# Kernel optimization log

Measured on AMD Instinct MI355X. Metric: run time of the kernel, lower is better.

The kernel has to match this reference:

```python
import jax, jax.numpy as jnp
import numpy as np

NUM_CAPSULE = 32
DIM_CAPSULE = 32
ROUTINGS = 3
T_EPSILON = 1e-7


def setup_inputs() -> dict:
    key = jax.random.key(0)
    k1, k2 = jax.random.split(key)
    x = jax.random.normal(k1, (64, 1024, 256), dtype=jnp.float32)
    # xavier_normal_ on [1, 256, 32*32]: std = sqrt(2/(fan_in+fan_out)) = sqrt(2/(256+1024))
    std = np.sqrt(2.0 / (256 + NUM_CAPSULE * DIM_CAPSULE)).astype(np.float32)
    W = jax.random.normal(k2, (1, 256, NUM_CAPSULE * DIM_CAPSULE), dtype=jnp.float32) * std
    return {"x": x, "W": W}


def _squash(v, eps):
    # x / sqrt(sum(x^2) + eps)  (note: not the classic squash; faithful to source)
    s = jnp.sum(v * v, axis=-1, keepdims=True)
    return v / jnp.sqrt(s + eps)


def reference(x, W):
    B, N_in, _ = x.shape
    # u_hat: [B, num_capsule, input_num_capsule, dim_capsule]
    u_hat = jnp.matmul(x, W).reshape(B, N_in, NUM_CAPSULE, DIM_CAPSULE)
    u_hat = jnp.transpose(u_hat, (0, 2, 1, 3))
    b = jnp.zeros(u_hat.shape[:3], dtype=u_hat.dtype)  # [B, num, n_in]
    outputs = None
    for i in range(ROUTINGS):
        # original: softmax over the num_capsule axis (dim=2 after permute(0,2,1))
        c = jax.nn.softmax(b, axis=1)  # [B, num, n_in]
        outputs = _squash(jnp.einsum('bij,bijk->bik', c, u_hat), T_EPSILON)  # [B, num, dim]
        if i < ROUTINGS - 1:
            b = jnp.einsum('bik,bijk->bij', outputs, u_hat)
    return outputs
```

## Files before the change

### kernel.cpp

```cpp
#include <hip/hip_runtime.h>
#include <cstdint>
#include <cstddef>

#define BATCH 64
#define NIN   1024
#define CIN   256
#define NC    32
#define NJC   16
#define JCH   64
#define T_EPS 1e-7f
#define CT_S  72

typedef __attribute__((ext_vector_type(8))) short short8;
typedef __attribute__((ext_vector_type(4))) float floatx4;

__device__ __forceinline__ unsigned short bf16rne(float f) {
  unsigned int u = __float_as_uint(f);
  u += 0x7FFFu + ((u >> 16) & 1u);
  return (unsigned short)(u >> 16);
}
__device__ __forceinline__ float bf2f(unsigned short h) {
  return __uint_as_float(((unsigned int)h) << 16);
}
__device__ __forceinline__ int xsw(int j, int c) {
  return j * 256 + ((((c >> 3) ^ (j & 7) ^ ((j >> 3) & 7)) << 3) | (c & 7));
}

__global__ __launch_bounds__(256) void k_convert(const float* __restrict__ x,
                                                 const float* __restrict__ W,
                                                 unsigned short* __restrict__ xb,
                                                 unsigned short* __restrict__ Wi,
                                                 float* __restrict__ y0p) {
  const int jc = blockIdx.x, b = blockIdx.y, t = threadIdx.x;
  const int jj = t >> 6, c4 = t & 63;
  __shared__ float4 red[4][64];
  const float4* xg = (const float4*)(x + ((size_t)(b * NIN + jc * JCH)) * CIN);
  ushort4* xo = (ushort4*)(xb + ((size_t)(b * NIN + jc * JCH)) * CIN);
  float4 acc = make_float4(0.f, 0.f, 0.f, 0.f);
  #pragma unroll
  for (int jr = 0; jr < 16; ++jr) {
    int j = jr * 4 + jj;
    float4 v = xg[j * 64 + c4];
    acc.x += v.x; acc.y += v.y; acc.z += v.z; acc.w += v.w;
    ushort4 h;
    h.x = bf16rne(v.x); h.y = bf16rne(v.y);
    h.z = bf16rne(v.z); h.w = bf16rne(v.w);
    xo[j * 64 + c4] = h;
  }
  red[jj][c4] = acc;
  if (b == 0) {
    #pragma unroll
    for (int i2 = 0; i2 < 2; ++i2) {
      int i = jc * 2 + i2;
      const float4* wsrc = (const float4*)(W + (size_t)t * 1024 + i * 32);
      unsigned short* wdst = Wi + ((size_t)i * CIN + t) * NC;
      #pragma unroll
      for (int k4 = 0; k4 < 8; ++k4) {
        float4 v = wsrc[k4];
        ushort4 h;
        h.x = bf16rne(v.x); h.y = bf16rne(v.y);
        h.z = bf16rne(v.z); h.w = bf16rne(v.w);
        *(ushort4*)&wdst[k4 * 4] = h;
      }
    }
  }
  __syncthreads();
  if (t < 64) {
    float4 s = red[0][t];
    #pragma unroll
    for (int p = 1; p < 4; ++p) {
      s.x += red[p][t].x; s.y += red[p][t].y;
      s.z += red[p][t].z; s.w += red[p][t].w;
    }
    *(float4*)&y0p[(b * NJC + jc) * CIN + t * 4] = s;
  }
}

template <int MODE>
__global__ __launch_bounds__(256) void k_post(const void* __restrict__ yin,
                                              const unsigned short* __restrict__ Wi,
                                              unsigned short* __restrict__ wtout,
                                              float* __restrict__ outg) {
  const int i = blockIdx.x, b = blockIdx.y, t = threadIdx.x;
  __shared__ float ys[CIN];
  __shared__ float sred[8][32];
  __shared__ float os[NC];
  float a = 0.f;
  if (MODE == 0) {
    const float* y0p = (const float*)yin;
    #pragma unroll
    for (int p = 0; p < NJC; ++p) a += y0p[(b * NJC + p) * CIN + t];
    a *= (1.f / 32.f);
  } else {
    const unsigned short* yp = (const unsigned short*)yin;
    #pragma unroll
    for (int p = 0; p < NJC; ++p)
      a += bf2f(yp[(((size_t)(b * NJC + p)) * NC + i) * CIN + t]);
  }
  ys[t] = a;
  __syncthreads();
  const unsigned short* Wis = Wi + (size_t)i * CIN * NC;
  {
    const int k = t & 31, g = t >> 5;
    float ps = 0.f;
    #pragma unroll
    for (int cc = 0; cc < 32; ++cc) {
      int c = g * 32 + ((cc + g * 4) & 31);
      ps += ys[c] * bf2f(Wis[c * NC + k]);
    }
    sred[g][k] = ps;
  }
  __syncthreads();
  const int k = t & 31;
  float s = 0.f;
  #pragma unroll
  for (int g = 0; g < 8; ++g) s += sred[g][k];
  float s2 = s * s;
  #pragma unroll
  for (int m = 1; m < 32; m <<= 1) s2 += __shfl_xor(s2, m);
  float o = s * rsqrtf(s2 + T_EPS);
  if (MODE == 2) {
    if (t < 32) outg[((size_t)b * NC + i) * 32 + t] = o;
  } else {
    if (t < 32) os[t] = o;
    __syncthreads();
    float acc = 0.f;
    const short8* wrow = (const short8*)(Wis + (size_t)t * NC);
    #pragma unroll
    for (int k8 = 0; k8 < 4; ++k8) {
      short8 wv = wrow[k8];
      #pragma unroll
      for (int e = 0; e < 8; ++e)
        acc += os[k8 * 8 + e] * bf2f((unsigned short)wv[e]);
    }
    wtout[((size_t)b * NC + i) * CIN + t] = bf16rne(acc);
  }
}

__global__ __launch_bounds__(256, 4) void k_fused(const unsigned short* __restrict__ xb,
                                                  const unsigned short* __restrict__ wt,
                                                  unsigned short* __restrict__ ypart) {
  const int jc = blockIdx.x, b = blockIdx.y, t = threadIdx.x;
  const int w = t >> 6, l16 = t & 15, q = (t >> 4) & 3;
  __shared__ unsigned short xs[64 * 256];
  __shared__ unsigned short cT[NC * CT_S];
  {
    const short8* xg =
        (const short8*)(xb + ((size_t)(b * NIN) + (size_t)jc * JCH) * CIN);
    #pragma unroll
    for (int it = 0; it < 8; ++it) {
      int f = it * 256 + t;
      int j = f >> 5, ch = f & 31;
      *(short8*)&xs[xsw(j, ch * 8)] = xg[f];
    }
  }
  const int jloc = w * 16 + l16;
  const unsigned short* wrow = wt + (size_t)b * NC * CIN;
  floatx4 accA0 = {0.f, 0.f, 0.f, 0.f}, accA1 = {0.f, 0.f, 0.f, 0.f};
  __syncthreads();
  #pragma unroll
  for (int ks = 0; ks < 8; ++ks) {
    short8 bx = *(const short8*)&xs[xsw(jloc, ks * 32 + q * 8)];
    short8 a0 = *(const short8*)(wrow + (size_t)l16 * CIN + ks * 32 + q * 8);
    short8 a1 = *(const short8*)(wrow + (size_t)(16 + l16) * CIN + ks * 32 + q * 8);
    accA0 = __builtin_amdgcn_mfma_f32_16x16x32_bf16(a0, bx, accA0, 0, 0, 0);
    accA1 = __builtin_amdgcn_mfma_f32_16x16x32_bf16(a1, bx, accA1, 0, 0, 0);
  }
  {
    float m = accA0[0];
    #pragma unroll
    for (int r = 1; r < 4; ++r) m = fmaxf(m, accA0[r]);
    #pragma unroll
    for (int r = 0; r < 4; ++r) m = fmaxf(m, accA1[r]);
    m = fmaxf(m, __shfl_xor(m, 16));
    m = fmaxf(m, __shfl_xor(m, 32));
    float e0[4], e1[4], s = 0.f;
    #pragma unroll
    for (int r = 0; r < 4; ++r) {
      e0[r] = __expf(accA0[r] - m);
      e1[r] = __expf(accA1[r] - m);
      s += e0[r] + e1[r];
    }
    s += __shfl_xor(s, 16);
    s += __shfl_xor(s, 32);
    float rs = 1.f / s;
    #pragma unroll
    for (int r = 0; r < 4; ++r) {
      cT[(q * 4 + r) * CT_S + jloc]      = bf16rne(e0[r] * rs);
      cT[(16 + q * 4 + r) * CT_S + jloc] = bf16rne(e1[r] * rs);
    }
  }
  __syncthreads();
  const int cw = w * 64;
  floatx4 accB[2][4];
  #pragma unroll
  for (int h = 0; h < 2; ++h)
    #pragma unroll
    for (int ct = 0; ct < 4; ++ct) accB[h][ct] = (floatx4){0.f, 0.f, 0.f, 0.f};
  #pragma unroll
  for (int ks = 0; ks < 2; ++ks) {
    short8 ca0 = *(const short8*)&cT[l16 * CT_S + ks * 32 + q * 8];
    short8 ca1 = *(const short8*)&cT[(16 + l16) * CT_S + ks * 32 + q * 8];
    #pragma unroll
    for (int ct = 0; ct < 4; ++ct) {
      const int c = cw + ct * 16 + l16;
      short8 xf;
      #pragma unroll
      for (int e = 0; e < 8; ++e)
        xf[e] = (short)xs[xsw(ks * 32 + q * 8 + e, c)];
      accB[0][ct] = __builtin_amdgcn_mfma_f32_16x16x32_bf16(ca0, xf, accB[0][ct], 0, 0, 0);
      accB[1][ct] = __builtin_amdgcn_mfma_f32_16x16x32_bf16(ca1, xf, accB[1][ct], 0, 0, 0);
    }
  }
  unsigned short* yo = ypart + ((size_t)(b * NJC + jc)) * NC * CIN;
  #pragma unroll
  for (int h = 0; h < 2; ++h)
    #pragma unroll
    for (int ct = 0; ct < 4; ++ct)
      #pragma unroll
      for (int r = 0; r < 4; ++r) {
        int i = h * 16 + q * 4 + r;
        int c = cw + ct * 16 + l16;
        yo[i * CIN + c] = bf16rne(accB[h][ct][r]);
      }
}

extern "C" void kernel_launch(void* const* d_in, const int* in_sizes, int n_in,
                              void* d_out, int out_size, void* d_ws, size_t ws_size,
                              hipStream_t stream) {
  (void)in_sizes; (void)n_in; (void)out_size; (void)ws_size;
  const float* x = (const float*)d_in[0];
  const float* W = (const float*)d_in[1];
  float* out = (float*)d_out;
  char* ws = (char*)d_ws;
  unsigned short* xbuf  = (unsigned short*)ws;
  unsigned short* wtb   = (unsigned short*)(ws + (32ull << 20));
  unsigned short* ypart = (unsigned short*)(ws + (33ull << 20));
  float*          y0p   = (float*)(ws + (49ull << 20));
  unsigned short* Wi    = (unsigned short*)(ws + (50ull << 20));

  dim3 gfuse(NJC, BATCH);
  dim3 gpost(NC, BATCH);
  k_convert<<<gfuse, 256, 0, stream>>>(x, W, xbuf, Wi, y0p);
  k_post<0><<<gpost, 256, 0, stream>>>(y0p, Wi, wtb, nullptr);
  k_fused<<<gfuse, 256, 0, stream>>>(xbuf, wtb, ypart);
  k_post<1><<<gpost, 256, 0, stream>>>(ypart, Wi, wtb, nullptr);
  k_fused<<<gfuse, 256, 0, stream>>>(xbuf, wtb, ypart);
  k_post<2><<<gpost, 256, 0, stream>>>(ypart, Wi, nullptr, out);
}
```

Baseline: 153.9 us.

## Fuse routing into one cooperative kernel keeping x resident in LDS

The six-launch pipeline is replaced by a single cooperative kernel with four blocks per batch. Each block converts its quarter of x to bf16 once and keeps it in shared memory for both routing iterations. The four blocks of a batch sync through global atomic counters, and partial sums go through workspace buffers. This removes the intermediate bf16 round-trips of x and the launch gaps. In exchange it runs one four-wave block per CU with low occupancy, each block redundantly converts a W slice, and the old path stays as a fallback if the cooperative launch fails.

```diff
diff --git a/kernel.cpp b/kernel.cpp
--- a/kernel.cpp
+++ b/kernel.cpp
@@ -10,6 +10,7 @@
 #define JCH   64
 #define T_EPS 1e-7f
 #define CT_S  72
+#define SCOPE_AGENT __HIP_MEMORY_SCOPE_AGENT
 
 typedef __attribute__((ext_vector_type(8))) short short8;
 typedef __attribute__((ext_vector_type(4))) float floatx4;
@@ -24,6 +25,386 @@
 }
 __device__ __forceinline__ int xsw(int j, int c) {
   return j * 256 + ((((c >> 3) ^ (j & 7) ^ ((j >> 3) & 7)) << 3) | (c & 7));
+}
+__device__ __forceinline__ int wsw(int i, int c) {
+  return i * 256 + ((((c >> 3) ^ (i & 7)) << 3) | (c & 7));
+}
+
+__device__ __forceinline__ float cload(const float* p) {
+  return __hip_atomic_load(p, __ATOMIC_RELAXED, SCOPE_AGENT);
+}
+__device__ __forceinline__ void cstore(float* p, float v) {
+  __hip_atomic_store(p, v, __ATOMIC_RELAXED, SCOPE_AGENT);
+}
+__device__ __forceinline__ unsigned int cloadu(const unsigned int* p) {
+  return __hip_atomic_load(p, __ATOMIC_RELAXED, SCOPE_AGENT);
+}
+__device__ __forceinline__ void cstoreu(unsigned int* p, unsigned int v) {
+  __hip_atomic_store(p, v, __ATOMIC_RELAXED, SCOPE_AGENT);
+}
+
+struct K2S { float ys[CIN]; float sred[8][32]; float os[NC]; };
+struct SQS { float ys2[8][CIN]; float os2[8][NC]; };
+union USH {
+  float4 red[4][64];
+  unsigned short cT[NC * CT_S];
+  K2S k2;
+  SQS sq;
+};
+
+__device__ __forceinline__ void groupbar(unsigned int* flag, unsigned int target,
+                                         int t) {
+  __syncthreads();
+  if (t == 0) {
+    __hip_atomic_fetch_add(flag, 1u, __ATOMIC_RELEASE, SCOPE_AGENT);
+    while (__hip_atomic_load(flag, __ATOMIC_RELAXED, SCOPE_AGENT) < target)
+      __builtin_amdgcn_s_sleep(2);
+    (void)__hip_atomic_load(flag, __ATOMIC_ACQUIRE, SCOPE_AGENT);
+  }
+  __syncthreads();
+}
+
+__device__ __forceinline__ void jloop_iter(int t, const unsigned short* xs,
+                                           const unsigned short* wts, USH& u,
+                                           floatx4 accB[2][4]) {
+  const int w = t >> 6, l16 = t & 15, q = (t >> 4) & 3;
+  const int jloc = w * 16 + l16;
+  #pragma unroll 1
+  for (int tile = 0; tile < 4; ++tile) {
+    const unsigned short* xt = xs + tile * 16384;
+    floatx4 accA0 = {0.f, 0.f, 0.f, 0.f}, accA1 = {0.f, 0.f, 0.f, 0.f};
+    #pragma unroll
+    for (int ks = 0; ks < 8; ++ks) {
+      short8 bx = *(const short8*)&xt[xsw(jloc, ks * 32 + q * 8)];
+      short8 a0 = *(const short8*)&wts[wsw(l16, ks * 32 + q * 8)];
+      short8 a1 = *(const short8*)&wts[wsw(16 + l16, ks * 32 + q * 8)];
+      accA0 = __builtin_amdgcn_mfma_f32_16x16x32_bf16(a0, bx, accA0, 0, 0, 0);
+      accA1 = __builtin_amdgcn_mfma_f32_16x16x32_bf16(a1, bx, accA1, 0, 0, 0);
+    }
+    {
+      float m = accA0[0];
+      #pragma unroll
+      for (int r = 1; r < 4; ++r) m = fmaxf(m, accA0[r]);
+      #pragma unroll
+      for (int r = 0; r < 4; ++r) m = fmaxf(m, accA1[r]);
+      m = fmaxf(m, __shfl_xor(m, 16));
+      m = fmaxf(m, __shfl_xor(m, 32));
+      float e0[4], e1[4], s = 0.f;
+      #pragma unroll
+      for (int r = 0; r < 4; ++r) {
+        e0[r] = __expf(accA0[r] - m);
+        e1[r] = __expf(accA1[r] - m);
+        s += e0[r] + e1[r];
+      }
+      s += __shfl_xor(s, 16);
+      s += __shfl_xor(s, 32);
+      float rs = 1.f / s;
+      #pragma unroll
+      for (int r = 0; r < 4; ++r) {
+        u.cT[(q * 4 + r) * CT_S + jloc]      = bf16rne(e0[r] * rs);
+        u.cT[(16 + q * 4 + r) * CT_S + jloc] = bf16rne(e1[r] * rs);
+      }
+    }
+    __syncthreads();
+    const int cw = w * 64;
+    #pragma unroll
+    for (int ks = 0; ks < 2; ++ks) {
+      short8 ca0 = *(const short8*)&u.cT[l16 * CT_S + ks * 32 + q * 8];
+      short8 ca1 = *(const short8*)&u.cT[(16 + l16) * CT_S + ks * 32 + q * 8];
+      #pragma unroll
+      for (int ct = 0; ct < 4; ++ct) {
+        const int c = cw + ct * 16 + l16;
+        short8 xf;
+        #pragma unroll
+        for (int e = 0; e < 8; ++e)
+          xf[e] = (short)xt[xsw(ks * 32 + q * 8 + e, c)];
+        accB[0][ct] = __builtin_amdgcn_mfma_f32_16x16x32_bf16(ca0, xf, accB[0][ct], 0, 0, 0);
+        accB[1][ct] = __builtin_amdgcn_mfma_f32_16x16x32_bf16(ca1, xf, accB[1][ct], 0, 0, 0);
+      }
+    }
+    __syncthreads();
+  }
+}
+
+template <bool LAST>
+__device__ __forceinline__ void squash_phase(int qb, int b, int t,
+                                             const unsigned short* __restrict__ Wi2,
+                                             unsigned int* __restrict__ wtx,
+                                             float* __restrict__ outg, USH& u) {
+  const int il = t >> 5, k = t & 31;
+  float o;
+  {
+    const unsigned short* wrow = Wi2 + ((size_t)(qb * 256 + t)) * CIN;
+    float s = 0.f;
+    #pragma unroll 8
+    for (int c8 = 0; c8 < 32; ++c8) {
+      short8 wv = *(const short8*)&wrow[c8 * 8];
+      #pragma unroll
+      for (int e = 0; e < 8; ++e)
+        s += u.sq.ys2[il][c8 * 8 + e] * bf2f((unsigned short)wv[e]);
+    }
+    float s2 = s * s;
+    #pragma unroll
+    for (int m = 1; m < 32; m <<= 1) s2 += __shfl_xor(s2, m);
+    o = s * rsqrtf(s2 + T_EPS);
+  }
+  if (LAST) {
+    outg[((size_t)b * NC + qb * 8 + il) * 32 + k] = o;
+    return;
+  }
+  u.sq.os2[il][k] = o;
+  __syncthreads();
+  {
+    float a[8];
+    #pragma unroll
+    for (int e = 0; e < 8; ++e) a[e] = 0.f;
+    const unsigned short* wbase = Wi2 + ((size_t)(qb * 256 + il * 32)) * CIN + k * 8;
+    #pragma unroll 8
+    for (int kk = 0; kk < 32; ++kk) {
+      short8 wv = *(const short8*)&wbase[(size_t)kk * CIN];
+      float ok = u.sq.os2[il][kk];
+      #pragma unroll
+      for (int e = 0; e < 8; ++e) a[e] += ok * bf2f((unsigned short)wv[e]);
+    }
+    unsigned int* dst = wtx + (((size_t)b * NC + qb * 8 + il) * CIN + k * 8) / 2;
+    #pragma unroll
+    for (int m2 = 0; m2 < 4; ++m2)
+      cstoreu(dst + m2, (unsigned int)bf16rne(a[2 * m2]) |
+                        ((unsigned int)bf16rne(a[2 * m2 + 1]) << 16));
+  }
+}
+
+__device__ __forceinline__ void load_wts(int b, int t,
+                                         const unsigned int* __restrict__ wtx,
+                                         unsigned short* wts) {
+  const int i = t >> 3, cb = (t & 7) * 32;
+  const unsigned int* src = wtx + ((size_t)b * NC + i) * (CIN / 2) + cb / 2;
+  #pragma unroll
+  for (int m = 0; m < 4; ++m) {
+    unsigned int v0 = cloadu(src + m * 4 + 0);
+    unsigned int v1 = cloadu(src + m * 4 + 1);
+    unsigned int v2 = cloadu(src + m * 4 + 2);
+    unsigned int v3 = cloadu(src + m * 4 + 3);
+    *(uint4*)&wts[wsw(i, cb + m * 8)] = make_uint4(v0, v1, v2, v3);
+  }
+}
+
+__global__ __launch_bounds__(256, 1) void k_one(const float* __restrict__ x,
+                                                const float* __restrict__ W,
+                                                unsigned short* __restrict__ Wi2,
+                                                float* __restrict__ csx,
+                                                float* __restrict__ ypx,
+                                                unsigned int* __restrict__ wtx,
+                                                unsigned int* __restrict__ flags,
+                                                float* __restrict__ outg) {
+  const int qb = blockIdx.x, b = blockIdx.y, t = threadIdx.x;
+  const int w = t >> 6;
+  __shared__ unsigned short xs[4 * 16384];
+  __shared__ unsigned short wts[NC * CIN];
+  __shared__ USH u;
+
+  {
+    unsigned short* wdst = Wi2 + ((size_t)(qb * 256 + t)) * CIN;
+    #pragma unroll 4
+    for (int c0 = 0; c0 < 32; ++c0) {
+      short8 h;
+      #pragma unroll
+      for (int e = 0; e < 8; ++e)
+        h[e] = (short)bf16rne(W[(size_t)(c0 * 8 + e) * 1024 + qb * 256 + t]);
+      *(short8*)&wdst[c0 * 8] = h;
+    }
+  }
+  {
+    const float4* xg = (const float4*)(x + ((size_t)b * NIN + qb * 256) * CIN);
+    const int c4 = t & 63;
+    float4 acc = make_float4(0.f, 0.f, 0.f, 0.f);
+    #pragma unroll 8
+    for (int it = 0; it < 64; ++it) {
+      int j = it * 4 + w;
+      float4 v = xg[(size_t)j * 64 + c4];
+      acc.x += v.x; acc.y += v.y; acc.z += v.z; acc.w += v.w;
+      ushort4 h;
+      h.x = bf16rne(v.x); h.y = bf16rne(v.y);
+      h.z = bf16rne(v.z); h.w = bf16rne(v.w);
+      *(ushort4*)&xs[(j >> 6) * 16384 + xsw(j & 63, c4 * 4)] = h;
+    }
+    u.red[w][c4] = acc;
+    __syncthreads();
+    if (t < 64) {
+      float4 s = u.red[0][t];
+      #pragma unroll
+      for (int p = 1; p < 4; ++p) {
+        s.x += u.red[p][t].x; s.y += u.red[p][t].y;
+        s.z += u.red[p][t].z; s.w += u.red[p][t].w;
+      }
+      float* dst = csx + ((size_t)b * 4 + qb) * CIN + t * 4;
+      cstore(dst + 0, s.x); cstore(dst + 1, s.y);
+      cstore(dst + 2, s.z); cstore(dst + 3, s.w);
+    }
+  }
+  groupbar(flags + b, 4u * 1u, t);
+
+  {
+    float v = 0.f;
+    #pragma unroll
+    for (int q2 = 0; q2 < 4; ++q2)
+      v += cload(&csx[((size_t)b * 4 + q2) * CIN + t]);
+    v *= (1.f / 32.f);
+    #pragma unroll
+    for (int il = 0; il < 8; ++il) u.sq.ys2[il][t] = v;
+  }
+  __syncthreads();
+  squash_phase<false>(qb, b, t, Wi2, wtx, nullptr, u);
+  groupbar(flags + b, 4u * 2u, t);
+
+  load_wts(b, t, wtx, wts);
+  __syncthreads();
+  {
+    floatx4 accB[2][4];
+    #pragma unroll
+    for (int h = 0; h < 2; ++h)
+      #pragma unroll
+      for (int ct = 0; ct < 4; ++ct) accB[h][ct] = (floatx4){0.f, 0.f, 0.f, 0.f};
+    jloop_iter(t, xs, wts, u, accB);
+    const int l16 = t & 15, q = (t >> 4) & 3;
+    #pragma unroll
+    for (int h = 0; h < 2; ++h)
+      #pragma unroll
+      for (int ct = 0; ct < 4; ++ct)
+        #pragma unroll
+        for (int r = 0; r < 4; ++r) {
+          int i = h * 16 + q * 4 + r;
+          int c = w * 64 + ct * 16 + l16;
+          cstore(&ypx[(((size_t)b * 4 + qb) * NC + i) * CIN + c], accB[h][ct][r]);
+        }
+  }
+  groupbar(flags + b, 4u * 3u, t);
+  {
+    #pragma unroll
+    for (int il = 0; il < 8; ++il) {
+      int i = qb * 8 + il;
+      float v = 0.f;
+      #pragma unroll
+      for (int q2 = 0; q2 < 4; ++q2)
+        v += cload(&ypx[(((size_t)b * 4 + q2) * NC + i) * CIN + t]);
+      u.sq.ys2[il][t] = v;
+    }
+  }
+  __syncthreads();
+  squash_phase<false>(qb, b, t, Wi2, wtx, nullptr, u);
+  groupbar(flags + b, 4u * 4u, t);
+
+  load_wts(b, t, wtx, wts);
+  __syncthreads();
+  {
+    floatx4 accB[2][4];
+    #pragma unroll
+    for (int h = 0; h < 2; ++h)
+      #pragma unroll
+      for (int ct = 0; ct < 4; ++ct) accB[h][ct] = (floatx4){0.f, 0.f, 0.f, 0.f};
+    jloop_iter(t, xs, wts, u, accB);
+    const int l16 = t & 15, q = (t >> 4) & 3;
+    #pragma unroll
+    for (int h = 0; h < 2; ++h)
+      #pragma unroll
+      for (int ct = 0; ct < 4; ++ct)
+        #pragma unroll
+        for (int r = 0; r < 4; ++r) {
+          int i = h * 16 + q * 4 + r;
+          int c = w * 64 + ct * 16 + l16;
+          cstore(&ypx[(((size_t)b * 4 + qb) * NC + i) * CIN + c], accB[h][ct][r]);
+        }
+  }
+  groupbar(flags + b, 4u * 5u, t);
+  {
+    #pragma unroll
+    for (int il = 0; il < 8; ++il) {
+      int i = qb * 8 + il;
+      float v = 0.f;
+      #pragma unroll
+      for (int q2 = 0; q2 < 4; ++q2)
+        v += cload(&ypx[(((size_t)b * 4 + q2) * NC + i) * CIN + t]);
+      u.sq.ys2[il][t] = v;
+    }
+  }
+  __syncthreads();
+  squash_phase<true>(qb, b, t, Wi2, nullptr, outg, u);
+}
+
+
+__device__ __forceinline__ void fused_iter_old(int b, int t,
+                                               const unsigned short* xs, USH* u,
+                                               const unsigned short* __restrict__ wt,
+                                               unsigned short* __restrict__ yo) {
+  const int w = t >> 6, l16 = t & 15, q = (t >> 4) & 3;
+  const int jloc = w * 16 + l16;
+  const unsigned short* wrow = wt + (size_t)b * NC * CIN;
+  floatx4 accA0 = {0.f, 0.f, 0.f, 0.f}, accA1 = {0.f, 0.f, 0.f, 0.f};
+  #pragma unroll
+  for (int ks = 0; ks < 8; ++ks) {
+    short8 bx = *(const short8*)&xs[xsw(jloc, ks * 32 + q * 8)];
+    short8 a0 = *(const short8*)(wrow + (size_t)l16 * CIN + ks * 32 + q * 8);
+    short8 a1 = *(const short8*)(wrow + (size_t)(16 + l16) * CIN + ks * 32 + q * 8);
+    accA0 = __builtin_amdgcn_mfma_f32_16x16x32_bf16(a0, bx, accA0, 0, 0, 0);
+    accA1 = __builtin_amdgcn_mfma_f32_16x16x32_bf16(a1, bx, accA1, 0, 0, 0);
+  }
+  {
+    float m = accA0[0];
+    #pragma unroll
+    for (int r = 1; r < 4; ++r) m = fmaxf(m, accA0[r]);
+    #pragma unroll
+    for (int r = 0; r < 4; ++r) m = fmaxf(m, accA1[r]);
+    m = fmaxf(m, __shfl_xor(m, 16));
+    m = fmaxf(m, __shfl_xor(m, 32));
+    float e0[4], e1[4], s = 0.f;
+    #pragma unroll
+    for (int r = 0; r < 4; ++r) {
+      e0[r] = __expf(accA0[r] - m);
+      e1[r] = __expf(accA1[r] - m);
+      s += e0[r] + e1[r];
+    }
+    s += __shfl_xor(s, 16);
+    s += __shfl_xor(s, 32);
+    float rs = 1.f / s;
+    #pragma unroll
+    for (int r = 0; r < 4; ++r) {
+      u->cT[(q * 4 + r) * CT_S + jloc]      = bf16rne(e0[r] * rs);
+      u->cT[(16 + q * 4 + r) * CT_S + jloc] = bf16rne(e1[r] * rs);
+    }
+  }
+  __syncthreads();
+  const int cw = w * 64;
+  floatx4 accB[2][4];
+  #pragma unroll
+  for (int h = 0; h < 2; ++h)
+    #pragma unroll
+    for (int ct = 0; ct < 4; ++ct) accB[h][ct] = (floatx4){0.f, 0.f, 0.f, 0.f};
+  #pragma unroll
+  for (int ks = 0; ks < 2; ++ks) {
+    short8 ca0 = *(const short8*)&u->cT[l16 * CT_S + ks * 32 + q * 8];
+    short8 ca1 = *(const short8*)&u->cT[(16 + l16) * CT_S + ks * 32 + q * 8];
+    #pragma unroll
+    for (int ct = 0; ct < 4; ++ct) {
+      const int c = cw + ct * 16 + l16;
+      short8 xf;
+      #pragma unroll
+      for (int e = 0; e < 8; ++e)
+        xf[e] = (short)xs[xsw(ks * 32 + q * 8 + e, c)];
+      accB[0][ct] = __builtin_amdgcn_mfma_f32_16x16x32_bf16(ca0, xf, accB[0][ct], 0, 0, 0);
+      accB[1][ct] = __builtin_amdgcn_mfma_f32_16x16x32_bf16(ca1, xf, accB[1][ct], 0, 0, 0);
+    }
+  }
+  #pragma unroll
+  for (int h = 0; h < 2; ++h)
+    #pragma unroll
+    for (int ct = 0; ct < 4; ++ct)
+      #pragma unroll
+      for (int r = 0; r < 4; ++r) {
+        int i = h * 16 + q * 4 + r;
+        int c = cw + ct * 16 + l16;
+        yo[i * CIN + c] = bf16rne(accB[h][ct][r]);
+      }
+  __syncthreads();
 }
 
 __global__ __launch_bounds__(256) void k_convert(const float* __restrict__ x,
@@ -141,9 +522,8 @@
                                                   const unsigned short* __restrict__ wt,
                                                   unsigned short* __restrict__ ypart) {
   const int jc = blockIdx.x, b = blockIdx.y, t = threadIdx.x;
-  const int w = t >> 6, l16 = t & 15, q = (t >> 4) & 3;
   __shared__ unsigned short xs[64 * 256];
-  __shared__ unsigned short cT[NC * CT_S];
+  __shared__ USH u;
   {
     const short8* xg =
         (const short8*)(xb + ((size_t)(b * NIN) + (size_t)jc * JCH) * CIN);
@@ -154,76 +534,10 @@
       *(short8*)&xs[xsw(j, ch * 8)] = xg[f];
     }
   }
-  const int jloc = w * 16 + l16;
-  const unsigned short* wrow = wt + (size_t)b * NC * CIN;
-  floatx4 accA0 = {0.f, 0.f, 0.f, 0.f}, accA1 = {0.f, 0.f, 0.f, 0.f};
-  __syncthreads();
-  #pragma unroll
-  for (int ks = 0; ks < 8; ++ks) {
-    short8 bx = *(const short8*)&xs[xsw(jloc, ks * 32 + q * 8)];
-    short8 a0 = *(const short8*)(wrow + (size_t)l16 * CIN + ks * 32 + q * 8);
-    short8 a1 = *(const short8*)(wrow + (size_t)(16 + l16) * CIN + ks * 32 + q * 8);
-    accA0 = __builtin_amdgcn_mfma_f32_16x16x32_bf16(a0, bx, accA0, 0, 0, 0);
-    accA1 = __builtin_amdgcn_mfma_f32_16x16x32_bf16(a1, bx, accA1, 0, 0, 0);
-  }
-  {
-    float m = accA0[0];
-    #pragma unroll
-    for (int r = 1; r < 4; ++r) m = fmaxf(m, accA0[r]);
-    #pragma unroll
-    for (int r = 0; r < 4; ++r) m = fmaxf(m, accA1[r]);
-    m = fmaxf(m, __shfl_xor(m, 16));
-    m = fmaxf(m, __shfl_xor(m, 32));
-    float e0[4], e1[4], s = 0.f;
-    #pragma unroll
-    for (int r = 0; r < 4; ++r) {
-      e0[r] = __expf(accA0[r] - m);
-      e1[r] = __expf(accA1[r] - m);
-      s += e0[r] + e1[r];
-    }
-    s += __shfl_xor(s, 16);
-    s += __shfl_xor(s, 32);
-    float rs = 1.f / s;
-    #pragma unroll
-    for (int r = 0; r < 4; ++r) {
-      cT[(q * 4 + r) * CT_S + jloc]      = bf16rne(e0[r] * rs);
-      cT[(16 + q * 4 + r) * CT_S + jloc] = bf16rne(e1[r] * rs);
-    }
-  }
-  __syncthreads();
-  const int cw = w * 64;
-  floatx4 accB[2][4];
-  #pragma unroll
-  for (int h = 0; h < 2; ++h)
-    #pragma unroll
-    for (int ct = 0; ct < 4; ++ct) accB[h][ct] = (floatx4){0.f, 0.f, 0.f, 0.f};
-  #pragma unroll
-  for (int ks = 0; ks < 2; ++ks) {
-    short8 ca0 = *(const short8*)&cT[l16 * CT_S + ks * 32 + q * 8];
-    short8 ca1 = *(const short8*)&cT[(16 + l16) * CT_S + ks * 32 + q * 8];
-    #pragma unroll
-    for (int ct = 0; ct < 4; ++ct) {
-      const int c = cw + ct * 16 + l16;
-      short8 xf;
-      #pragma unroll
-      for (int e = 0; e < 8; ++e)
-        xf[e] = (short)xs[xsw(ks * 32 + q * 8 + e, c)];
-      accB[0][ct] = __builtin_amdgcn_mfma_f32_16x16x32_bf16(ca0, xf, accB[0][ct], 0, 0, 0);
-      accB[1][ct] = __builtin_amdgcn_mfma_f32_16x16x32_bf16(ca1, xf, accB[1][ct], 0, 0, 0);
-    }
-  }
-  unsigned short* yo = ypart + ((size_t)(b * NJC + jc)) * NC * CIN;
-  #pragma unroll
-  for (int h = 0; h < 2; ++h)
-    #pragma unroll
-    for (int ct = 0; ct < 4; ++ct)
-      #pragma unroll
-      for (int r = 0; r < 4; ++r) {
-        int i = h * 16 + q * 4 + r;
-        int c = cw + ct * 16 + l16;
-        yo[i * CIN + c] = bf16rne(accB[h][ct][r]);
-      }
-}
+  __syncthreads();
+  fused_iter_old(b, t, xs, &u, wt, ypart + ((size_t)(b * NJC + jc)) * NC * CIN);
+}
+
 
 extern "C" void kernel_launch(void* const* d_in, const int* in_sizes, int n_in,
                               void* d_out, int out_size, void* d_ws, size_t ws_size,
@@ -233,18 +547,41 @@
   const float* W = (const float*)d_in[1];
   float* out = (float*)d_out;
   char* ws = (char*)d_ws;
-  unsigned short* xbuf  = (unsigned short*)ws;
-  unsigned short* wtb   = (unsigned short*)(ws + (32ull << 20));
-  unsigned short* ypart = (unsigned short*)(ws + (33ull << 20));
-  float*          y0p   = (float*)(ws + (49ull << 20));
-  unsigned short* Wi    = (unsigned short*)(ws + (50ull << 20));
-
-  dim3 gfuse(NJC, BATCH);
-  dim3 gpost(NC, BATCH);
-  k_convert<<<gfuse, 256, 0, stream>>>(x, W, xbuf, Wi, y0p);
-  k_post<0><<<gpost, 256, 0, stream>>>(y0p, Wi, wtb, nullptr);
-  k_fused<<<gfuse, 256, 0, stream>>>(xbuf, wtb, ypart);
-  k_post<1><<<gpost, 256, 0, stream>>>(ypart, Wi, wtb, nullptr);
-  k_fused<<<gfuse, 256, 0, stream>>>(xbuf, wtb, ypart);
-  k_post<2><<<gpost, 256, 0, stream>>>(ypart, Wi, nullptr, out);
-}
+
+  unsigned short* Wi2  = (unsigned short*)ws;
+  float*          csx  = (float*)(ws + (1ull << 20));
+  float*          ypx  = (float*)(ws + (2ull << 20));
+  unsigned int*   wtx  = (unsigned int*)(ws + (10ull << 20));
+  unsigned int*   flags = (unsigned int*)(ws + (11ull << 20));
+
+  (void)hipMemsetAsync(flags, 0, BATCH * sizeof(unsigned int), stream);
+
+  const float* xa = x;
+  const float* Wa = W;
+  unsigned short* Wi2a = Wi2;
+  float* csxa = csx;
+  float* ypxa = ypx;
+  unsigned int* wtxa = wtx;
+  unsigned int* flagsa = flags;
+  float* outa = out;
+  void* args[] = {(void*)&xa, (void*)&Wa, (void*)&Wi2a, (void*)&csxa,
+                  (void*)&ypxa, (void*)&wtxa, (void*)&flagsa, (void*)&outa};
+  hipError_t e = hipLaunchCooperativeKernel((const void*)k_one, dim3(4, BATCH),
+                                            dim3(256), args, 0, stream);
+  if (e != hipSuccess) {
+    (void)hipGetLastError();
+    unsigned short* xbuf  = (unsigned short*)ws;
+    unsigned short* wtb   = (unsigned short*)(ws + (32ull << 20));
+    unsigned short* ypart = (unsigned short*)(ws + (33ull << 20));
+    float*          y0p   = (float*)(ws + (49ull << 20));
+    unsigned short* Wi    = (unsigned short*)(ws + (50ull << 20));
+    dim3 gfuse(NJC, BATCH);
+    dim3 gpost(NC, BATCH);
+    k_convert<<<gfuse, 256, 0, stream>>>(x, W, xbuf, Wi, y0p);
+    k_post<0><<<gpost, 256, 0, stream>>>(y0p, Wi, wtb, nullptr);
+    k_fused<<<gfuse, 256, 0, stream>>>(xbuf, wtb, ypart);
+    k_post<1><<<gpost, 256, 0, stream>>>(ypart, Wi, wtb, nullptr);
+    k_fused<<<gfuse, 256, 0, stream>>>(xbuf, wtb, ypart);
+    k_post<2><<<gpost, 256, 0, stream>>>(ypart, Wi, nullptr, out);
+  }
+}
```

Result: slower. 235.3 us (+52.9%).

## Fold per-batch post-processing into last-arriving block via atomic counters

Applied to the files above, without the earlier changes.

Removes the three separate k_post launches by having the last of the 16 blocks per batch (detected with an agent-scope atomic counter) run the reduction, squash and W-projection inline. W is reformatted by a separate small kernel into two layouts suited to the tail's vectorized reads, and partial y outputs are packed as bf16 pairs with relaxed atomic stores. This cuts launch count and inter-kernel gaps. In exchange, one block per batch does 32 capsules of serial tail work, and a memset of the counters is added.

```diff
diff --git a/kernel.cpp b/kernel.cpp
--- a/kernel.cpp
+++ b/kernel.cpp
@@ -10,6 +10,7 @@
 #define JCH   64
 #define T_EPS 1e-7f
 #define CT_S  72
+#define SCOPE_AGENT __HIP_MEMORY_SCOPE_AGENT
 
 typedef __attribute__((ext_vector_type(8))) short short8;
 typedef __attribute__((ext_vector_type(4))) float floatx4;
@@ -26,14 +27,120 @@
   return j * 256 + ((((c >> 3) ^ (j & 7) ^ ((j >> 3) & 7)) << 3) | (c & 7));
 }
 
-__global__ __launch_bounds__(256) void k_convert(const float* __restrict__ x,
-                                                 const float* __restrict__ W,
-                                                 unsigned short* __restrict__ xb,
-                                                 unsigned short* __restrict__ Wi,
-                                                 float* __restrict__ y0p) {
+__device__ __forceinline__ float cload(const float* p) {
+  return __hip_atomic_load(p, __ATOMIC_RELAXED, SCOPE_AGENT);
+}
+__device__ __forceinline__ void cstore(float* p, float v) {
+  __hip_atomic_store(p, v, __ATOMIC_RELAXED, SCOPE_AGENT);
+}
+__device__ __forceinline__ unsigned int cloadu(const unsigned int* p) {
+  return __hip_atomic_load(p, __ATOMIC_RELAXED, SCOPE_AGENT);
+}
+__device__ __forceinline__ void cstoreu(unsigned int* p, unsigned int v) {
+  __hip_atomic_store(p, v, __ATOMIC_RELAXED, SCOPE_AGENT);
+}
+
+struct TPS { float ys2[8][CIN]; float os2[8][NC]; };
+union USH { unsigned short cT[NC * CT_S]; };
+
+__global__ __launch_bounds__(256) void k_wbuild(const float* __restrict__ W,
+                                                unsigned short* __restrict__ Wq,
+                                                unsigned short* __restrict__ Wp) {
+  const int i = blockIdx.x, t = threadIdx.x;
+  const float4* wsrc = (const float4*)(W + (size_t)t * 1024 + i * 32);
+  const int slice = (i >> 3) * 4 + ((i >> 1) & 3);
+  const int il2 = i & 1;
+  unsigned short* qb = Wq + (size_t)slice * 16384 + (t >> 3) * 512 + (t & 7);
+  #pragma unroll
+  for (int k8 = 0; k8 < 4; ++k8) {
+    float4 v0 = wsrc[k8 * 2], v1 = wsrc[k8 * 2 + 1];
+    unsigned short h[8] = {bf16rne(v0.x), bf16rne(v0.y), bf16rne(v0.z), bf16rne(v0.w),
+                           bf16rne(v1.x), bf16rne(v1.y), bf16rne(v1.z), bf16rne(v1.w)};
+    short8 pv;
+    #pragma unroll
+    for (int e = 0; e < 8; ++e) {
+      int k = k8 * 8 + e;
+      qb[(il2 * 32 + k) * 8] = h[e];
+      pv[e] = (short)h[e];
+    }
+    *(short8*)&Wp[(((size_t)i * 4 + k8) * CIN + t) * 8] = pv;
+  }
+}
+
+template <int MODE>
+__device__ __forceinline__ void tail_post(int b, int t,
+    const float* __restrict__ y0p, const unsigned int* __restrict__ yp32,
+    const unsigned short* __restrict__ Wq, const unsigned short* __restrict__ Wp,
+    unsigned short* __restrict__ wtb, float* __restrict__ outg, TPS* tp) {
+  const int w = t >> 6, lane = t & 63, il = t >> 5, k = t & 31;
+  if (MODE == 0) {
+    float a = 0.f;
+    #pragma unroll
+    for (int p = 0; p < NJC; ++p) a += cload(&y0p[(b * NJC + p) * CIN + t]);
+    tp->ys2[0][t] = a * (1.f / 32.f);
+  }
+  #pragma unroll 1
+  for (int g4 = 0; g4 < 4; ++g4) {
+    if (MODE != 0) {
+      #pragma unroll 1
+      for (int l = 0; l < 8; ++l) {
+        float a = 0.f;
+        #pragma unroll
+        for (int p = 0; p < NJC; ++p) {
+          unsigned int v =
+              cloadu(&yp32[(((size_t)(b * NJC + p)) * NC + g4 * 8 + l) * 128 + (t >> 1)]);
+          a += bf2f((unsigned short)((t & 1) ? (v >> 16) : (v & 0xffffu)));
+        }
+        tp->ys2[l][t] = a;
+      }
+    }
+    __syncthreads();
+    {
+      const float* ysrow = (MODE == 0) ? tp->ys2[0] : tp->ys2[il];
+      const short8* wq = (const short8*)Wq + ((size_t)(g4 * 4 + w)) * 2048 + lane;
+      float s = 0.f;
+      #pragma unroll 8
+      for (int c8 = 0; c8 < 32; ++c8) {
+        short8 wv = wq[c8 * 64];
+        #pragma unroll
+        for (int e = 0; e < 8; ++e) s += ysrow[c8 * 8 + e] * bf2f((unsigned short)wv[e]);
+      }
+      float s2 = s * s;
+      #pragma unroll
+      for (int m = 1; m < 32; m <<= 1) s2 += __shfl_xor(s2, m);
+      float o = s * rsqrtf(s2 + T_EPS);
+      if (MODE == 2) outg[((size_t)b * NC + g4 * 8 + il) * 32 + k] = o;
+      else tp->os2[il][k] = o;
+    }
+    __syncthreads();
+    if (MODE != 2) {
+      #pragma unroll 1
+      for (int l = 0; l < 8; ++l) {
+        int i = g4 * 8 + l;
+        float acc = 0.f;
+        #pragma unroll
+        for (int k8 = 0; k8 < 4; ++k8) {
+          short8 wv = *((const short8*)Wp + ((size_t)i * 4 + k8) * CIN + t);
+          #pragma unroll
+          for (int e = 0; e < 8; ++e)
+            acc += tp->os2[l][k8 * 8 + e] * bf2f((unsigned short)wv[e]);
+        }
+        wtb[((size_t)b * NC + i) * CIN + t] = bf16rne(acc);
+      }
+      __syncthreads();
+    }
+  }
+}
+
+__global__ __launch_bounds__(256) void k_convA(const float* __restrict__ x,
+    unsigned short* __restrict__ xb, float* __restrict__ y0p,
+    const unsigned short* __restrict__ Wq, const unsigned short* __restrict__ Wp,
+    unsigned short* __restrict__ wtb, unsigned int* __restrict__ dc) {
   const int jc = blockIdx.x, b = blockIdx.y, t = threadIdx.x;
   const int jj = t >> 6, c4 = t & 63;
-  __shared__ float4 red[4][64];
+  union ALDS { float4 red[4][64]; TPS tp; };
+  __shared__ ALDS s_;
+  __shared__ int lastf;
   const float4* xg = (const float4*)(x + ((size_t)(b * NIN + jc * JCH)) * CIN);
   ushort4* xo = (ushort4*)(xb + ((size_t)(b * NIN + jc * JCH)) * CIN);
   float4 acc = make_float4(0.f, 0.f, 0.f, 0.f);
@@ -47,111 +154,46 @@
     h.z = bf16rne(v.z); h.w = bf16rne(v.w);
     xo[j * 64 + c4] = h;
   }
-  red[jj][c4] = acc;
-  if (b == 0) {
-    #pragma unroll
-    for (int i2 = 0; i2 < 2; ++i2) {
-      int i = jc * 2 + i2;
-      const float4* wsrc = (const float4*)(W + (size_t)t * 1024 + i * 32);
-      unsigned short* wdst = Wi + ((size_t)i * CIN + t) * NC;
-      #pragma unroll
-      for (int k4 = 0; k4 < 8; ++k4) {
-        float4 v = wsrc[k4];
-        ushort4 h;
-        h.x = bf16rne(v.x); h.y = bf16rne(v.y);
-        h.z = bf16rne(v.z); h.w = bf16rne(v.w);
-        *(ushort4*)&wdst[k4 * 4] = h;
-      }
-    }
-  }
+  s_.red[jj][c4] = acc;
   __syncthreads();
   if (t < 64) {
-    float4 s = red[0][t];
+    float4 s = s_.red[0][t];
     #pragma unroll
     for (int p = 1; p < 4; ++p) {
-      s.x += red[p][t].x; s.y += red[p][t].y;
-      s.z += red[p][t].z; s.w += red[p][t].w;
-    }
-    *(float4*)&y0p[(b * NJC + jc) * CIN + t * 4] = s;
-  }
-}
-
-template <int MODE>
-__global__ __launch_bounds__(256) void k_post(const void* __restrict__ yin,
-                                              const unsigned short* __restrict__ Wi,
-                                              unsigned short* __restrict__ wtout,
-                                              float* __restrict__ outg) {
-  const int i = blockIdx.x, b = blockIdx.y, t = threadIdx.x;
-  __shared__ float ys[CIN];
-  __shared__ float sred[8][32];
-  __shared__ float os[NC];
-  float a = 0.f;
-  if (MODE == 0) {
-    const float* y0p = (const float*)yin;
-    #pragma unroll
-    for (int p = 0; p < NJC; ++p) a += y0p[(b * NJC + p) * CIN + t];
-    a *= (1.f / 32.f);
-  } else {
-    const unsigned short* yp = (const unsigned short*)yin;
-    #pragma unroll
-    for (int p = 0; p < NJC; ++p)
-      a += bf2f(yp[(((size_t)(b * NJC + p)) * NC + i) * CIN + t]);
-  }
-  ys[t] = a;
-  __syncthreads();
-  const unsigned short* Wis = Wi + (size_t)i * CIN * NC;
-  {
-    const int k = t & 31, g = t >> 5;
-    float ps = 0.f;
-    #pragma unroll
-    for (int cc = 0; cc < 32; ++cc) {
-      int c = g * 32 + ((cc + g * 4) & 31);
-      ps += ys[c] * bf2f(Wis[c * NC + k]);
-    }
-    sred[g][k] = ps;
-  }
-  __syncthreads();
-  const int k = t & 31;
-  float s = 0.f;
-  #pragma unroll
-  for (int g = 0; g < 8; ++g) s += sred[g][k];
-  float s2 = s * s;
-  #pragma unroll
-  for (int m = 1; m < 32; m <<= 1) s2 += __shfl_xor(s2, m);
-  float o = s * rsqrtf(s2 + T_EPS);
-  if (MODE == 2) {
-    if (t < 32) outg[((size_t)b * NC + i) * 32 + t] = o;
-  } else {
-    if (t < 32) os[t] = o;
-    __syncthreads();
-    float acc = 0.f;
-    const short8* wrow = (const short8*)(Wis + (size_t)t * NC);
-    #pragma unroll
-    for (int k8 = 0; k8 < 4; ++k8) {
-      short8 wv = wrow[k8];
-      #pragma unroll
-      for (int e = 0; e < 8; ++e)
-        acc += os[k8 * 8 + e] * bf2f((unsigned short)wv[e]);
-    }
-    wtout[((size_t)b * NC + i) * CIN + t] = bf16rne(acc);
-  }
-}
-
-__global__ __launch_bounds__(256, 4) void k_fused(const unsigned short* __restrict__ xb,
-                                                  const unsigned short* __restrict__ wt,
-                                                  unsigned short* __restrict__ ypart) {
+      s.x += s_.red[p][t].x; s.y += s_.red[p][t].y;
+      s.z += s_.red[p][t].z; s.w += s_.red[p][t].w;
+    }
+    float* dst = y0p + ((size_t)(b * NJC + jc)) * CIN + t * 4;
+    cstore(dst + 0, s.x); cstore(dst + 1, s.y);
+    cstore(dst + 2, s.z); cstore(dst + 3, s.w);
+  }
+  __syncthreads();
+  if (t == 0)
+    lastf = (__hip_atomic_fetch_add(&dc[b], 1u, __ATOMIC_ACQ_REL, SCOPE_AGENT) == NJC - 1);
+  __syncthreads();
+  if (!lastf) return;
+  tail_post<0>(b, t, y0p, nullptr, Wq, Wp, wtb, nullptr, &s_.tp);
+}
+
+template <int FM>
+__global__ __launch_bounds__(256, 4) void k_fusedm(const unsigned short* __restrict__ xb,
+    const unsigned short* __restrict__ wt, unsigned int* __restrict__ yp32,
+    const unsigned short* __restrict__ Wq, const unsigned short* __restrict__ Wp,
+    unsigned short* __restrict__ wtout, float* __restrict__ outg,
+    unsigned int* __restrict__ dc) {
   const int jc = blockIdx.x, b = blockIdx.y, t = threadIdx.x;
   const int w = t >> 6, l16 = t & 15, q = (t >> 4) & 3;
-  __shared__ unsigned short xs[64 * 256];
-  __shared__ unsigned short cT[NC * CT_S];
+  union FLDS { unsigned short xs[64 * 256]; TPS tp; };
+  __shared__ FLDS sm;
+  __shared__ USH u;
+  __shared__ int lastf;
   {
-    const short8* xg =
-        (const short8*)(xb + ((size_t)(b * NIN) + (size_t)jc * JCH) * CIN);
+    const short8* xg = (const short8*)(xb + ((size_t)(b * NIN) + (size_t)jc * JCH) * CIN);
     #pragma unroll
     for (int it = 0; it < 8; ++it) {
-      int f = it * 256 + t;
-      int j = f >> 5, ch = f & 31;
-      *(short8*)&xs[xsw(j, ch * 8)] = xg[f];
+      int fi = it * 256 + t;
+      int j = fi >> 5, ch = fi & 31;
+      *(short8*)&sm.xs[xsw(j, ch * 8)] = xg[fi];
     }
   }
   const int jloc = w * 16 + l16;
@@ -160,7 +202,7 @@
   __syncthreads();
   #pragma unroll
   for (int ks = 0; ks < 8; ++ks) {
-    short8 bx = *(const short8*)&xs[xsw(jloc, ks * 32 + q * 8)];
+    short8 bx = *(const short8*)&sm.xs[xsw(jloc, ks * 32 + q * 8)];
     short8 a0 = *(const short8*)(wrow + (size_t)l16 * CIN + ks * 32 + q * 8);
     short8 a1 = *(const short8*)(wrow + (size_t)(16 + l16) * CIN + ks * 32 + q * 8);
     accA0 = __builtin_amdgcn_mfma_f32_16x16x32_bf16(a0, bx, accA0, 0, 0, 0);
@@ -186,8 +228,8 @@
     float rs = 1.f / s;
     #pragma unroll
     for (int r = 0; r < 4; ++r) {
-      cT[(q * 4 + r) * CT_S + jloc]      = bf16rne(e0[r] * rs);
-      cT[(16 + q * 4 + r) * CT_S + jloc] = bf16rne(e1[r] * rs);
+      u.cT[(q * 4 + r) * CT_S + jloc]      = bf16rne(e0[r] * rs);
+      u.cT[(16 + q * 4 + r) * CT_S + jloc] = bf16rne(e1[r] * rs);
     }
   }
   __syncthreads();
@@ -199,31 +241,42 @@
     for (int ct = 0; ct < 4; ++ct) accB[h][ct] = (floatx4){0.f, 0.f, 0.f, 0.f};
   #pragma unroll
   for (int ks = 0; ks < 2; ++ks) {
-    short8 ca0 = *(const short8*)&cT[l16 * CT_S + ks * 32 + q * 8];
-    short8 ca1 = *(const short8*)&cT[(16 + l16) * CT_S + ks * 32 + q * 8];
+    short8 ca0 = *(const short8*)&u.cT[l16 * CT_S + ks * 32 + q * 8];
+    short8 ca1 = *(const short8*)&u.cT[(16 + l16) * CT_S + ks * 32 + q * 8];
     #pragma unroll
     for (int ct = 0; ct < 4; ++ct) {
       const int c = cw + ct * 16 + l16;
       short8 xf;
       #pragma unroll
       for (int e = 0; e < 8; ++e)
-        xf[e] = (short)xs[xsw(ks * 32 + q * 8 + e, c)];
+        xf[e] = (short)sm.xs[xsw(ks * 32 + q * 8 + e, c)];
       accB[0][ct] = __builtin_amdgcn_mfma_f32_16x16x32_bf16(ca0, xf, accB[0][ct], 0, 0, 0);
       accB[1][ct] = __builtin_amdgcn_mfma_f32_16x16x32_bf16(ca1, xf, accB[1][ct], 0, 0, 0);
     }
   }
-  unsigned short* yo = ypart + ((size_t)(b * NJC + jc)) * NC * CIN;
   #pragma unroll
   for (int h = 0; h < 2; ++h)
     #pragma unroll
     for (int ct = 0; ct < 4; ++ct)
       #pragma unroll
       for (int r = 0; r < 4; ++r) {
-        int i = h * 16 + q * 4 + r;
-        int c = cw + ct * 16 + l16;
-        yo[i * CIN + c] = bf16rne(accB[h][ct][r]);
+        float fv = accB[h][ct][r];
+        float gv = __shfl_xor(fv, 1);
+        if ((l16 & 1) == 0) {
+          int i = h * 16 + q * 4 + r;
+          int c = cw + ct * 16 + l16;
+          cstoreu(&yp32[(((size_t)(b * NJC + jc)) * NC + i) * 128 + (c >> 1)],
+                  (unsigned int)bf16rne(fv) | ((unsigned int)bf16rne(gv) << 16));
+        }
       }
-}
+  __syncthreads();
+  if (t == 0)
+    lastf = (__hip_atomic_fetch_add(&dc[b], 1u, __ATOMIC_ACQ_REL, SCOPE_AGENT) == NJC - 1);
+  __syncthreads();
+  if (!lastf) return;
+  tail_post<FM>(b, t, nullptr, yp32, Wq, Wp, wtout, outg, &sm.tp);
+}
+
 
 extern "C" void kernel_launch(void* const* d_in, const int* in_sizes, int n_in,
                               void* d_out, int out_size, void* d_ws, size_t ws_size,
@@ -233,18 +286,19 @@
   const float* W = (const float*)d_in[1];
   float* out = (float*)d_out;
   char* ws = (char*)d_ws;
-  unsigned short* xbuf  = (unsigned short*)ws;
-  unsigned short* wtb   = (unsigned short*)(ws + (32ull << 20));
-  unsigned short* ypart = (unsigned short*)(ws + (33ull << 20));
-  float*          y0p   = (float*)(ws + (49ull << 20));
-  unsigned short* Wi    = (unsigned short*)(ws + (50ull << 20));
-
-  dim3 gfuse(NJC, BATCH);
-  dim3 gpost(NC, BATCH);
-  k_convert<<<gfuse, 256, 0, stream>>>(x, W, xbuf, Wi, y0p);
-  k_post<0><<<gpost, 256, 0, stream>>>(y0p, Wi, wtb, nullptr);
-  k_fused<<<gfuse, 256, 0, stream>>>(xbuf, wtb, ypart);
-  k_post<1><<<gpost, 256, 0, stream>>>(ypart, Wi, wtb, nullptr);
-  k_fused<<<gfuse, 256, 0, stream>>>(xbuf, wtb, ypart);
-  k_post<2><<<gpost, 256, 0, stream>>>(ypart, Wi, nullptr, out);
-}
+  unsigned short* xb   = (unsigned short*)ws;
+  unsigned short* wtb  = (unsigned short*)(ws + (32ull << 20));
+  unsigned int*   yp32 = (unsigned int*)(ws + (33ull << 20));
+  float*          y0p  = (float*)(ws + (50ull << 20));
+  unsigned short* Wq   = (unsigned short*)(ws + (51ull << 20));
+  unsigned short* Wp   = (unsigned short*)(ws + (51ull << 20) + (512ull << 10));
+  unsigned int*   dcnt = (unsigned int*)(ws + (52ull << 20));
+
+  (void)hipMemsetAsync(dcnt, 0, 3 * BATCH * sizeof(unsigned int), stream);
+
+  dim3 g(NJC, BATCH);
+  k_wbuild<<<dim3(NC), 256, 0, stream>>>(W, Wq, Wp);
+  k_convA<<<g, 256, 0, stream>>>(x, xb, y0p, Wq, Wp, wtb, dcnt);
+  k_fusedm<1><<<g, 256, 0, stream>>>(xb, wtb, yp32, Wq, Wp, wtb, nullptr, dcnt + BATCH);
+  k_fusedm<2><<<g, 256, 0, stream>>>(xb, wtb, yp32, Wq, Wp, nullptr, out, dcnt + 2 * BATCH);
+}
```

New measurement: 377.4 us. +145.2%, slower.
